# Kernel optimization log

Measured on AMD Instinct MI355X. Metric: run time of the kernel, lower is better.

The kernel has to match this reference:

```python
import jax, jax.numpy as jnp
import numpy as np

EPS = 1e-5

def setup_inputs() -> dict:
    key = jax.random.key(0)
    k1, k2 = jax.random.split(key)
    N, C, B = 2000000, 32, 16
    data = jax.random.normal(k1, (N, C), dtype=jnp.float32)
    batch_id = jnp.sort(jax.random.randint(k2, (N,), 0, B, dtype=jnp.int32))
    weights = jnp.ones((1, C), dtype=jnp.float32)
    bias = jnp.zeros((1, C), dtype=jnp.float32)
    return {"data": data, "batch_id": batch_id, "batch_size": B,
            "weights": weights, "bias": bias}

def reference(data, batch_id, batch_size, weights, bias):
    # Per-octree (segment) instance norm over nodes, per channel.
    # count[b] = number of nodes in octree b
    ones = jnp.ones((data.shape[0], 1), dtype=data.dtype)
    count = jax.ops.segment_sum(ones, batch_id, num_segments=batch_size)  # [B,1]
    norm = 1.0 / (count + EPS)                                            # [B,1]
    mean = jax.ops.segment_sum(data, batch_id, num_segments=batch_size) * norm  # [B,C]
    out = data - mean[batch_id]                                           # [N,C]
    var = jax.ops.segment_sum(out * out, batch_id, num_segments=batch_size) * norm
    inv_std = 1.0 / jnp.sqrt(var + EPS)                                   # [B,C]
    out = out * inv_std[batch_id]
    return out * weights + bias
```

## Files before the change

### kernel.cpp

```cpp
#include <hip/hip_runtime.h>

#define EPS 1e-5f
#define NB 16
#define NC 32
#define NBLK 2048

__global__ __launch_bounds__(256) void oin_stats(
    const float* __restrict__ data,
    const int* __restrict__ batch_id,
    int N, int chunk,
    float* __restrict__ g_sum,
    float* __restrict__ g_sumsq,
    float* __restrict__ g_cnt)
{
    __shared__ float s_sum[NB * NC];
    __shared__ float s_sumsq[NB * NC];
    __shared__ float s_cnt[NB];

    for (int i = threadIdx.x; i < NB * NC; i += 256) { s_sum[i] = 0.f; s_sumsq[i] = 0.f; }
    if (threadIdx.x < NB) s_cnt[threadIdx.x] = 0.f;
    __syncthreads();

    const int c4    = threadIdx.x & 7;
    const int rlane = threadIdx.x >> 3;

    int start = blockIdx.x * chunk;
    int end   = start + chunk;
    if (end > N) end = N;

    if (start < N) {
        const float4* __restrict__ d4 = (const float4*)data;
        float4 a  = make_float4(0.f, 0.f, 0.f, 0.f);
        float4 a2 = make_float4(0.f, 0.f, 0.f, 0.f);
        float  cnt = 0.f;

        int b0 = batch_id[start];
        int b1 = batch_id[end - 1];

        if (b0 == b1) {
            int row = start + rlane;
            for (; row + 96 < end; row += 128) {
                float4 v0 = d4[row * 8 + c4];
                float4 v1 = d4[(row + 32) * 8 + c4];
                float4 v2 = d4[(row + 64) * 8 + c4];
                float4 v3 = d4[(row + 96) * 8 + c4];
                a.x += v0.x; a.y += v0.y; a.z += v0.z; a.w += v0.w;
                a2.x += v0.x*v0.x; a2.y += v0.y*v0.y; a2.z += v0.z*v0.z; a2.w += v0.w*v0.w;
                a.x += v1.x; a.y += v1.y; a.z += v1.z; a.w += v1.w;
                a2.x += v1.x*v1.x; a2.y += v1.y*v1.y; a2.z += v1.z*v1.z; a2.w += v1.w*v1.w;
                a.x += v2.x; a.y += v2.y; a.z += v2.z; a.w += v2.w;
                a2.x += v2.x*v2.x; a2.y += v2.y*v2.y; a2.z += v2.z*v2.z; a2.w += v2.w*v2.w;
                a.x += v3.x; a.y += v3.y; a.z += v3.z; a.w += v3.w;
                a2.x += v3.x*v3.x; a2.y += v3.y*v3.y; a2.z += v3.z*v3.z; a2.w += v3.w*v3.w;
                cnt += 4.f;
            }
            for (; row < end; row += 32) {
                float4 v = d4[row * 8 + c4];
                a.x += v.x; a.y += v.y; a.z += v.z; a.w += v.w;
                a2.x += v.x*v.x; a2.y += v.y*v.y; a2.z += v.z*v.z; a2.w += v.w*v.w;
                cnt += 1.f;
            }
            int base = b0 * NC + c4 * 4;
            atomicAdd(&s_sum[base + 0], a.x);  atomicAdd(&s_sum[base + 1], a.y);
            atomicAdd(&s_sum[base + 2], a.z);  atomicAdd(&s_sum[base + 3], a.w);
            atomicAdd(&s_sumsq[base + 0], a2.x); atomicAdd(&s_sumsq[base + 1], a2.y);
            atomicAdd(&s_sumsq[base + 2], a2.z); atomicAdd(&s_sumsq[base + 3], a2.w);
            if (c4 == 0) atomicAdd(&s_cnt[b0], cnt);
        } else {
            int cur = -1;
            for (int row = start + rlane; row < end; row += 32) {
                float4 v = d4[row * 8 + c4];
                int b = batch_id[row];
                if (b != cur) {
                    if (cur >= 0) {
                        int base = cur * NC + c4 * 4;
                        atomicAdd(&s_sum[base + 0], a.x);  atomicAdd(&s_sum[base + 1], a.y);
                        atomicAdd(&s_sum[base + 2], a.z);  atomicAdd(&s_sum[base + 3], a.w);
                        atomicAdd(&s_sumsq[base + 0], a2.x); atomicAdd(&s_sumsq[base + 1], a2.y);
                        atomicAdd(&s_sumsq[base + 2], a2.z); atomicAdd(&s_sumsq[base + 3], a2.w);
                        if (c4 == 0) atomicAdd(&s_cnt[cur], cnt);
                    }
                    cur = b;
                    a  = make_float4(0.f, 0.f, 0.f, 0.f);
                    a2 = make_float4(0.f, 0.f, 0.f, 0.f);
                    cnt = 0.f;
                }
                a.x += v.x; a.y += v.y; a.z += v.z; a.w += v.w;
                a2.x += v.x*v.x; a2.y += v.y*v.y; a2.z += v.z*v.z; a2.w += v.w*v.w;
                cnt += 1.f;
            }
            if (cur >= 0) {
                int base = cur * NC + c4 * 4;
                atomicAdd(&s_sum[base + 0], a.x);  atomicAdd(&s_sum[base + 1], a.y);
                atomicAdd(&s_sum[base + 2], a.z);  atomicAdd(&s_sum[base + 3], a.w);
                atomicAdd(&s_sumsq[base + 0], a2.x); atomicAdd(&s_sumsq[base + 1], a2.y);
                atomicAdd(&s_sumsq[base + 2], a2.z); atomicAdd(&s_sumsq[base + 3], a2.w);
                if (c4 == 0) atomicAdd(&s_cnt[cur], cnt);
            }
        }
    }
    __syncthreads();

    for (int i = threadIdx.x; i < NB * NC; i += 256) {
        float s = s_sum[i], q = s_sumsq[i];
        if (s != 0.f || q != 0.f) {
            atomicAdd(&g_sum[i], s);
            atomicAdd(&g_sumsq[i], q);
        }
    }
    if (threadIdx.x < NB) {
        float c = s_cnt[threadIdx.x];
        if (c != 0.f) atomicAdd(&g_cnt[threadIdx.x], c);
    }
}

__global__ __launch_bounds__(256) void oin_norm(
    const float* __restrict__ data,
    const int* __restrict__ batch_id,
    const float* __restrict__ g_sum,
    const float* __restrict__ g_sumsq,
    const float* __restrict__ g_cnt,
    const float* __restrict__ weights,
    const float* __restrict__ bias,
    float* __restrict__ out, int N, int chunk)
{
    __shared__ float4 s_sc[NB * NC / 4];
    __shared__ float4 s_sh[NB * NC / 4];
    {
        float* sc = (float*)s_sc;
        float* sh = (float*)s_sh;
        for (int t = threadIdx.x; t < NB * NC; t += 256) {
            int b = t >> 5, c = t & 31;
            float count = g_cnt[b];
            float norm  = 1.f / (count + EPS);
            float mean  = g_sum[t] * norm;
            float cn    = count * norm;
            float var   = g_sumsq[t] * norm - (2.f - cn) * mean * mean;
            float inv_std = 1.f / sqrtf(var + EPS);
            float scale = inv_std * weights[c];
            sc[t] = scale;
            sh[t] = bias[c] - mean * scale;
        }
    }
    __syncthreads();

    int start = blockIdx.x * chunk;
    int end   = start + chunk;
    if (end > N) end = N;
    if (start >= N) return;

    const float4* __restrict__ in4 = (const float4*)data;
    float4* __restrict__ out4 = (float4*)out;

    int e0 = start * 8;
    int e1 = end * 8;

    int b0 = batch_id[start];
    int b1 = batch_id[end - 1];

    if (b0 == b1) {
        float4 sc = s_sc[b0 * 8 + (threadIdx.x & 7)];
        float4 sh = s_sh[b0 * 8 + (threadIdx.x & 7)];

        int nfull  = (e1 - e0) >> 10;
        int remEnd = e1 - (nfull << 10);

        for (int base = e1 - 1024; base >= remEnd; base -= 1024) {
            int i = base + threadIdx.x;
            float4 v0 = in4[i];
            float4 v1 = in4[i + 256];
            float4 v2 = in4[i + 512];
            float4 v3 = in4[i + 768];
            float4 o0, o1, o2, o3;
            o0.x = v0.x*sc.x + sh.x; o0.y = v0.y*sc.y + sh.y; o0.z = v0.z*sc.z + sh.z; o0.w = v0.w*sc.w + sh.w;
            o1.x = v1.x*sc.x + sh.x; o1.y = v1.y*sc.y + sh.y; o1.z = v1.z*sc.z + sh.z; o1.w = v1.w*sc.w + sh.w;
            o2.x = v2.x*sc.x + sh.x; o2.y = v2.y*sc.y + sh.y; o2.z = v2.z*sc.z + sh.z; o2.w = v2.w*sc.w + sh.w;
            o3.x = v3.x*sc.x + sh.x; o3.y = v3.y*sc.y + sh.y; o3.z = v3.z*sc.z + sh.z; o3.w = v3.w*sc.w + sh.w;
            out4[i]       = o0;
            out4[i + 256] = o1;
            out4[i + 512] = o2;
            out4[i + 768] = o3;
        }
        for (int i = e0 + threadIdx.x; i < remEnd; i += 256) {
            float4 v = in4[i];
            float4 o;
            o.x = v.x*sc.x + sh.x; o.y = v.y*sc.y + sh.y; o.z = v.z*sc.z + sh.z; o.w = v.w*sc.w + sh.w;
            out4[i] = o;
        }
    } else {
        for (int i = e0 + threadIdx.x; i < e1; i += 256) {
            float4 v = in4[i];
            int b = batch_id[i >> 3];
            float4 sc = s_sc[b * 8 + (i & 7)];
            float4 sh = s_sh[b * 8 + (i & 7)];
            float4 o;
            o.x = v.x*sc.x + sh.x; o.y = v.y*sc.y + sh.y; o.z = v.z*sc.z + sh.z; o.w = v.w*sc.w + sh.w;
            out4[i] = o;
        }
    }
}

extern "C" void kernel_launch(void* const* d_in, const int* in_sizes, int n_in,
                              void* d_out, int out_size, void* d_ws, size_t ws_size,
                              hipStream_t stream) {
    const float* data     = (const float*)d_in[0];
    const int*   batch_id = (const int*)d_in[1];
    const float* weights  = (const float*)d_in[3];
    const float* bias     = (const float*)d_in[4];
    float* out = (float*)d_out;

    int N = in_sizes[0] / NC;

    float* g_sum   = (float*)d_ws;
    float* g_sumsq = g_sum + NB * NC;
    float* g_cnt   = g_sumsq + NB * NC;

    hipMemsetAsync(d_ws, 0, (size_t)(NB * NC * 2 + NB) * sizeof(float), stream);

    int chunk = (N + NBLK - 1) / NBLK;
    oin_stats<<<NBLK, 256, 0, stream>>>(data, batch_id, N, chunk, g_sum, g_sumsq, g_cnt);
    oin_norm<<<NBLK, 256, 0, stream>>>(data, batch_id, g_sum, g_sumsq, g_cnt,
                                       weights, bias, out, N, chunk);
}
```

Measured before the change: 499.6 us.

## Fuse stats and normalize kernels with a grid-wide atomic barrier

Merges the statistics and normalization kernels into one persistent kernel. Blocks spin on a global atomic counter until all have contributed their partial sums, then compute scale/shift and normalize their own chunk. Grid size is halved to 1024 with launch bounds of 4 blocks per CU so all blocks can be co-resident. This removes a kernel launch and may let the second read of each chunk hit in cache, at the risk of deadlock if not all blocks are resident and of idle time while blocks spin.

```diff
diff --git a/kernel.cpp b/kernel.cpp
--- a/kernel.cpp
+++ b/kernel.cpp
@@ -3,26 +3,32 @@
 #define EPS 1e-5f
 #define NB 16
 #define NC 32
-#define NBLK 2048
-
-__global__ __launch_bounds__(256) void oin_stats(
+#define NBLK 1024
+
+__global__ __launch_bounds__(256, 4) void oin_fused(
     const float* __restrict__ data,
     const int* __restrict__ batch_id,
+    const float* __restrict__ weights,
+    const float* __restrict__ bias,
+    float* __restrict__ out,
     int N, int chunk,
     float* __restrict__ g_sum,
     float* __restrict__ g_sumsq,
-    float* __restrict__ g_cnt)
+    float* __restrict__ g_cnt,
+    int* __restrict__ g_bar)
 {
     __shared__ float s_sum[NB * NC];
     __shared__ float s_sumsq[NB * NC];
     __shared__ float s_cnt[NB];
+    __shared__ float4 s_sc[NB * NC / 4];
+    __shared__ float4 s_sh[NB * NC / 4];
+
+    const int c4    = threadIdx.x & 7;
+    const int rlane = threadIdx.x >> 3;
 
     for (int i = threadIdx.x; i < NB * NC; i += 256) { s_sum[i] = 0.f; s_sumsq[i] = 0.f; }
     if (threadIdx.x < NB) s_cnt[threadIdx.x] = 0.f;
     __syncthreads();
-
-    const int c4    = threadIdx.x & 7;
-    const int rlane = threadIdx.x >> 3;
 
     int start = blockIdx.x * chunk;
     int end   = start + chunk;
@@ -112,30 +118,27 @@
         float c = s_cnt[threadIdx.x];
         if (c != 0.f) atomicAdd(&g_cnt[threadIdx.x], c);
     }
-}
-
-__global__ __launch_bounds__(256) void oin_norm(
-    const float* __restrict__ data,
-    const int* __restrict__ batch_id,
-    const float* __restrict__ g_sum,
-    const float* __restrict__ g_sumsq,
-    const float* __restrict__ g_cnt,
-    const float* __restrict__ weights,
-    const float* __restrict__ bias,
-    float* __restrict__ out, int N, int chunk)
-{
-    __shared__ float4 s_sc[NB * NC / 4];
-    __shared__ float4 s_sh[NB * NC / 4];
+
+    __syncthreads();
+    if (threadIdx.x == 0) {
+        __hip_atomic_fetch_add(g_bar, 1, __ATOMIC_RELEASE, __HIP_MEMORY_SCOPE_AGENT);
+        while (__hip_atomic_load(g_bar, __ATOMIC_ACQUIRE, __HIP_MEMORY_SCOPE_AGENT)
+               < (int)gridDim.x) { }
+    }
+    __syncthreads();
+
     {
         float* sc = (float*)s_sc;
         float* sh = (float*)s_sh;
         for (int t = threadIdx.x; t < NB * NC; t += 256) {
             int b = t >> 5, c = t & 31;
-            float count = g_cnt[b];
+            float count = __hip_atomic_load(&g_cnt[b],  __ATOMIC_RELAXED, __HIP_MEMORY_SCOPE_AGENT);
+            float sum   = __hip_atomic_load(&g_sum[t],  __ATOMIC_RELAXED, __HIP_MEMORY_SCOPE_AGENT);
+            float ssq   = __hip_atomic_load(&g_sumsq[t],__ATOMIC_RELAXED, __HIP_MEMORY_SCOPE_AGENT);
             float norm  = 1.f / (count + EPS);
-            float mean  = g_sum[t] * norm;
+            float mean  = sum * norm;
             float cn    = count * norm;
-            float var   = g_sumsq[t] * norm - (2.f - cn) * mean * mean;
+            float var   = ssq * norm - (2.f - cn) * mean * mean;
             float inv_std = 1.f / sqrtf(var + EPS);
             float scale = inv_std * weights[c];
             sc[t] = scale;
@@ -144,9 +147,6 @@
     }
     __syncthreads();
 
-    int start = blockIdx.x * chunk;
-    int end   = start + chunk;
-    if (end > N) end = N;
     if (start >= N) return;
 
     const float4* __restrict__ in4 = (const float4*)data;
@@ -159,8 +159,8 @@
     int b1 = batch_id[end - 1];
 
     if (b0 == b1) {
-        float4 sc = s_sc[b0 * 8 + (threadIdx.x & 7)];
-        float4 sh = s_sh[b0 * 8 + (threadIdx.x & 7)];
+        float4 sc = s_sc[b0 * 8 + c4];
+        float4 sh = s_sh[b0 * 8 + c4];
 
         int nfull  = (e1 - e0) >> 10;
         int remEnd = e1 - (nfull << 10);
@@ -214,11 +214,11 @@
     float* g_sum   = (float*)d_ws;
     float* g_sumsq = g_sum + NB * NC;
     float* g_cnt   = g_sumsq + NB * NC;
-
-    hipMemsetAsync(d_ws, 0, (size_t)(NB * NC * 2 + NB) * sizeof(float), stream);
+    int*   g_bar   = (int*)(g_cnt + NB);
+
+    hipMemsetAsync(d_ws, 0, 8192, stream);
 
     int chunk = (N + NBLK - 1) / NBLK;
-    oin_stats<<<NBLK, 256, 0, stream>>>(data, batch_id, N, chunk, g_sum, g_sumsq, g_cnt);
-    oin_norm<<<NBLK, 256, 0, stream>>>(data, batch_id, g_sum, g_sumsq, g_cnt,
-                                       weights, bias, out, N, chunk);
+    oin_fused<<<NBLK, 256, 0, stream>>>(data, batch_id, weights, bias, out,
+                                        N, chunk, g_sum, g_sumsq, g_cnt, g_bar);
 }
```

After: 776.1 us. +55.3%, slower.
